# Kernel optimization log

Hardware: AMD Instinct MI355X
Metric: run time of the kernel (lower is better)

## Reference

```python
import jax, jax.numpy as jnp
import numpy as np
from jax import lax

PAD = 10
K = 2 * PAD + 1  # 21
EPS = 1e-8


def _window(x, init, op):
    # sliding KxK window over the last two dims, stride 1, VALID
    return lax.reduce_window(x, init, op, (1, 1, K, K), (1, 1, 1, 1), 'VALID')


def setup_inputs() -> dict:
    key = jax.random.key(0)
    image = jax.random.uniform(key, (16, 3, 1024, 1024), dtype=jnp.float32)
    return {"image": image}


def reference(image):
    # replicate-pad by 2*PAD on each spatial side -> (B, C, H+4p, W+4p)
    padded = jnp.pad(image, ((0, 0), (0, 0), (2 * PAD, 2 * PAD), (2 * PAD, 2 * PAD)), mode='edge')
    # sliding-window min/max, output size (B, C, H+2p, W+2p)
    mn = _window(padded, jnp.inf, lax.min)      # = -maxpool(-padded)
    mx = _window(padded, -jnp.inf, lax.max)
    # Original computes mean over the KxK unfolded windows of
    #   (image - min_w) / (diff_w + eps)
    # which is linear in image:  image * mean(1/(diff+eps)) - mean(min/(diff+eps)).
    a = 1.0 / (mx - mn + EPS)
    b = mn * a
    inv_area = 1.0 / (K * K)
    avg_a = _window(a, 0.0, lax.add) * inv_area  # (B, C, H, W)
    avg_b = _window(b, 0.0, lax.add) * inv_area
    return image * avg_a - avg_b
```

## Files before the change

kernel.cpp:

```cpp
#include <hip/hip_runtime.h>

#define HDIM 1024
#define TILE 32
#define HALO 20
#define MID  52
#define ABW  1044
#define ABP2 1056
#define EPSF 1e-8f
#define INVF ((float)(1.0 / 441.0))

__device__ __forceinline__ void scan8_mm(const float* vm, const float* vx, float2* o) {
    float smn[8], smx[8];
    float amn = vm[20], amx = vx[20];
#pragma unroll
    for (int j = 19; j >= 8; --j) { amn = fminf(amn, vm[j]); amx = fmaxf(amx, vx[j]); }
#pragma unroll
    for (int i = 7; i >= 0; --i) {
        amn = fminf(amn, vm[i]); amx = fmaxf(amx, vx[i]);
        smn[i] = amn; smx[i] = amx;
    }
    float pmn = vm[21], pmx = vx[21];
    o[0] = make_float2(smn[0], smx[0]);
#pragma unroll
    for (int i = 1; i < 8; ++i) {
        o[i] = make_float2(fminf(smn[i], pmn), fmaxf(smx[i], pmx));
        if (i < 7) { pmn = fminf(pmn, vm[21 + i]); pmx = fmaxf(pmx, vx[21 + i]); }
    }
}

#define K1_IMG_PITCH 54
#define K1_HMM_OFF 4536
#define K1_HMM_PITCH 170
#define K1_WORDS 9984

__global__ __launch_bounds__(256, 4) void san_k1(const float* __restrict__ img,
                                                 float2* __restrict__ ab) {
    __shared__ __align__(16) float smem[K1_WORDS];
    const int tid = threadIdx.x;
    const int I0 = blockIdx.x * 32;
    const int J0 = blockIdx.y * 64;
    const float* __restrict__ imc = img + (size_t)blockIdx.z * (HDIM * HDIM);
    float2* __restrict__ abc = ab + (size_t)blockIdx.z * ((size_t)ABW * ABP2);
    const bool xInt = (blockIdx.x > 0) && (blockIdx.x < gridDim.x - 1);

    for (int idx = tid; idx < 84 * 26; idx += 256) {
        int r = idx / 26, c2 = idx - r * 26;
        int gy = min(HDIM - 1, max(0, J0 - HALO + r));
        float2 t;
        if (xInt) {
            t = *(const float2*)(imc + gy * HDIM + (I0 - HALO) + 2 * c2);
        } else {
            int gx0 = min(HDIM - 1, max(0, I0 - HALO + 2 * c2));
            int gx1 = min(HDIM - 1, max(0, I0 - HALO + 2 * c2 + 1));
            t = make_float2(imc[gy * HDIM + gx0], imc[gy * HDIM + gx1]);
        }
        *(float2*)&smem[r * K1_IMG_PITCH + 2 * c2] = t;
    }
    __syncthreads();

    for (int task = tid; task < 336; task += 256) {
        int r = task >> 2, g = task & 3;
        const float2* p = (const float2*)&smem[r * K1_IMG_PITCH + 8 * g];
        float v[28];
#pragma unroll
        for (int k = 0; k < 14; ++k) { float2 t = p[k]; v[2 * k] = t.x; v[2 * k + 1] = t.y; }
        float2 o[8];
        scan8_mm(v, v, o);
#pragma unroll
        for (int t = 0; t < 8; ++t)
            *(float2*)&smem[K1_HMM_OFF + (8 * g + t) * K1_HMM_PITCH + 2 * r] = o[t];
    }
    __syncthreads();

    {
        int i = tid & 31, gj = tid >> 5;
        const float2* p = (const float2*)&smem[K1_HMM_OFF + i * K1_HMM_PITCH + 16 * gj];
        float vm[28], vx[28];
#pragma unroll
        for (int k = 0; k < 28; ++k) { float2 t = p[k]; vm[k] = t.x; vx[k] = t.y; }
        float2 o[8];
        scan8_mm(vm, vx, o);
#pragma unroll
        for (int t = 0; t < 8; ++t) {
            int jj = J0 + 8 * gj + t, ii = I0 + i;
            float mn = o[t].x, d = o[t].y - o[t].x;
            float a, b;
            if (d == 0.0f) {
                a = 1.0f; b = 0.0f;
            } else {
                a = 1.0f / (d + EPSF);
                b = mn * a;
            }
            if (jj < ABW && ii < ABW)
                abc[(size_t)jj * ABP2 + ii] = make_float2(a, b);
        }
    }
}

#define K2_AB_PITCH 108
#define K2_HS_PITCH 106
#define K2_WORDS 5620

__global__ __launch_bounds__(256, 6) void san_k2(const float* __restrict__ img,
                                                 const float2* __restrict__ ab,
                                                 float* __restrict__ out) {
    __shared__ __align__(16) float smem[K2_WORDS];
    const int tid = threadIdx.x;
    const int I0 = blockIdx.x * TILE;
    const int J0 = blockIdx.y * TILE;
    const float* __restrict__ imc = img + (size_t)blockIdx.z * (HDIM * HDIM);
    const float2* __restrict__ abc = ab + (size_t)blockIdx.z * ((size_t)ABW * ABP2);
    float* __restrict__ oc = out + (size_t)blockIdx.z * (HDIM * HDIM);

    const int px_x = I0 + (tid & 31);
    const int px_y0 = J0 + 4 * (tid >> 5);
    float pix[4];
#pragma unroll
    for (int t = 0; t < 4; ++t) pix[t] = imc[(px_y0 + t) * HDIM + px_x];

    for (int idx = tid; idx < 52 * 26; idx += 256) {
        int r = idx / 26, c4 = idx - r * 26;
        const float4* gp = (const float4*)(abc + (size_t)(J0 + r) * ABP2 + I0) + c4;
        *(float4*)&smem[r * K2_AB_PITCH + 4 * c4] = *gp;
    }
    __syncthreads();

    const bool cornerBlk = (blockIdx.x == 0 || blockIdx.x == gridDim.x - 1) &&
                           (blockIdx.y == 0 || blockIdx.y == gridDim.y - 1);
    float fixVal = 0.0f;
    int fixPy = 0, fixPx = 0;
    float hsa[8], hsb[8];
    if (tid < 208) {
        int v = tid >> 2, g = tid & 3;
        const float4* p = (const float4*)&smem[v * K2_AB_PITCH + 16 * g];
        float2 abv[28];
#pragma unroll
        for (int k = 0; k < 14; ++k) {
            float4 q = p[k];
            abv[2 * k]     = make_float2(q.x, q.y);
            abv[2 * k + 1] = make_float2(q.z, q.w);
        }
        float Sa = 0.0f, Sb = 0.0f;
#pragma unroll
        for (int j = 0; j < 21; ++j) { Sa += abv[j].x; Sb += abv[j].y; }
        hsa[0] = Sa; hsb[0] = Sb;
#pragma unroll
        for (int t = 1; t < 8; ++t) {
            Sa += abv[t + 20].x - abv[t - 1].x;
            Sb += abv[t + 20].y - abv[t - 1].y;
            hsa[t] = Sa; hsb[t] = Sb;
        }
    } else if (cornerBlk && tid == 255) {
        fixPy = (blockIdx.y == 0) ? 0 : (TILE - 1);
        fixPx = (blockIdx.x == 0) ? 0 : (TILE - 1);
        int degY = (blockIdx.y == 0) ? 0 : HALO;
        int degX = (blockIdx.x == 0) ? 0 : HALO;
        float pv = imc[(J0 + fixPy) * HDIM + (I0 + fixPx)];
        float aT = 1.0f / EPSF;
        float bT = pv * aT;
        asm volatile("" : "+v"(bT));
        float Sa = 0.0f, Sb = 0.0f;
#pragma unroll 1
        for (int dy = 0; dy < 21; ++dy) {
#pragma unroll 1
            for (int dx = 0; dx < 21; ++dx) {
                const float* c = &smem[(fixPy + dy) * K2_AB_PITCH + 2 * (fixPx + dx)];
                float av = c[0], bv = c[1];
                if (dy == degY && dx == degX) { av = aT; bv = bT; }
                Sa = Sa + av;
                Sb = Sb + bv;
            }
        }
        float avga = Sa * INVF;
        float avgb = Sb * INVF;
        float tq = pv * avga;
        asm volatile("" : "+v"(tq));
        fixVal = tq - avgb;
    }
    __syncthreads();

    if (tid < 208) {
        int v = tid >> 2, g = tid & 3;
        int xp = 9 * g;
#pragma unroll
        for (int t = 0; t < 8; ++t)
            *(float2*)&smem[(xp + t) * K2_HS_PITCH + 2 * v] = make_float2(hsa[t], hsb[t]);
    }
    __syncthreads();

    {
        int x = tid & 31, h = tid >> 5, y0 = 4 * h;
        int xp = 9 * (x >> 3) + (x & 7);
        const float2* p = (const float2*)&smem[xp * K2_HS_PITCH] + y0;
        float2 vv[24];
#pragma unroll
        for (int j = 0; j < 24; ++j) vv[j] = p[j];
        float Sa = 0.0f, Sb = 0.0f;
#pragma unroll
        for (int j = 0; j < 21; ++j) { Sa += vv[j].x; Sb += vv[j].y; }
#pragma unroll
        for (int t = 0; t < 4; ++t) {
            if (t > 0) {
                Sa += vv[t + 20].x - vv[t - 1].x;
                Sb += vv[t + 20].y - vv[t - 1].y;
            }
            float avga = Sa * INVF, avgb = Sb * INVF;
            oc[(px_y0 + t) * HDIM + px_x] = pix[t] * avga - avgb;
        }
    }

    if (cornerBlk) {
        __syncthreads();
        if (tid == 255) oc[(J0 + fixPy) * HDIM + (I0 + fixPx)] = fixVal;
    }
}

#define IMG_PITCH 74
#define REG2 5616
#define HMM_STRIDE 148
#define AB_PITCH 108
#define HS_STRIDE 106
#define SMEM_WORDS 13328

__device__ __forceinline__ void scan14_mm(const float* vm, const float* vx, float2* o) {
    float smn[14], smx[14];
    float amn = vm[20], amx = vx[20];
#pragma unroll
    for (int j = 19; j >= 14; --j) { amn = fminf(amn, vm[j]); amx = fmaxf(amx, vx[j]); }
#pragma unroll
    for (int i = 13; i >= 0; --i) {
        amn = fminf(amn, vm[i]); amx = fmaxf(amx, vx[i]);
        smn[i] = amn; smx[i] = amx;
    }
    float pmn = vm[21], pmx = vx[21];
    o[0] = make_float2(smn[0], smx[0]);
#pragma unroll
    for (int i = 1; i < 14; ++i) {
        o[i] = make_float2(fminf(smn[i], pmn), fmaxf(smx[i], pmx));
        if (i < 13) { pmn = fminf(pmn, vm[21 + i]); pmx = fmaxf(pmx, vx[21 + i]); }
    }
}

__global__ __launch_bounds__(256, 3) void san_fused(const float* __restrict__ img,
                                                    float* __restrict__ out) {
    __shared__ __align__(16) float smem[SMEM_WORDS];
    const int tid = threadIdx.x;
    const int ox0 = blockIdx.x * TILE;
    const int oy0 = blockIdx.y * TILE;
    const float* __restrict__ imc = img + (size_t)blockIdx.z * (HDIM * HDIM);
    float* __restrict__ oc = out + (size_t)blockIdx.z * (HDIM * HDIM);
    const bool xInterior = (blockIdx.x > 0) && (blockIdx.x < gridDim.x - 1);

    for (int idx = tid; idx < 72 * 36; idx += 256) {
        int r = idx / 36, c2 = idx - r * 36;
        int gy = min(HDIM - 1, max(0, oy0 - HALO + r));
        float2 t;
        if (xInterior) {
            t = *(const float2*)(imc + gy * HDIM + (ox0 - HALO) + 2 * c2);
        } else {
            int gx0 = min(HDIM - 1, max(0, ox0 - HALO + 2 * c2));
            int gx1 = min(HDIM - 1, max(0, ox0 - HALO + 2 * c2 + 1));
            t = make_float2(imc[gy * HDIM + gx0], imc[gy * HDIM + gx1]);
        }
        *(float2*)&smem[r * IMG_PITCH + 2 * c2] = t;
    }
    __syncthreads();

    for (int task = tid; task < 288; task += 256) {
        int r = task >> 2, g = task & 3, u0 = 14 * g;
        const float2* p = (const float2*)&smem[r * IMG_PITCH + u0];
        float v[34];
#pragma unroll
        for (int k = 0; k < 17; ++k) { float2 t = p[k]; v[2 * k] = t.x; v[2 * k + 1] = t.y; }
        float2 o[14];
        scan14_mm(v, v, o);
#pragma unroll
        for (int i = 0; i < 14; ++i) {
            int u = u0 + i;
            if (u < MID) *(float2*)&smem[REG2 + u * HMM_STRIDE + 2 * r] = o[i];
        }
    }
    __syncthreads();

    if (tid < 208) {
        int u = tid % MID, v0 = 14 * (tid / MID);
        const float4* p = (const float4*)&smem[REG2 + u * HMM_STRIDE + 2 * v0];
        float vm[34], vx[34];
#pragma unroll
        for (int k = 0; k < 17; ++k) {
            float4 q = p[k];
            vm[2 * k] = q.x; vx[2 * k] = q.y; vm[2 * k + 1] = q.z; vx[2 * k + 1] = q.w;
        }
        float2 o[14];
        scan14_mm(vm, vx, o);
#pragma unroll
        for (int i = 0; i < 14; ++i) {
            int v = v0 + i;
            if (v < MID) {
                float mn = o[i].x, d = o[i].y - o[i].x;
                float a, b;
                if (d == 0.0f) { a = 1.0f; b = 0.0f; }
                else { a = 1.0f / (d + EPSF); b = mn * a; }
                *(float2*)&smem[v * AB_PITCH + 2 * u] = make_float2(a, b);
            }
        }
    }
    __syncthreads();

    const bool cornerBlk = (blockIdx.x == 0 || blockIdx.x == gridDim.x - 1) &&
                           (blockIdx.y == 0 || blockIdx.y == gridDim.y - 1);
    float fixVal = 0.0f;
    int fixPy = 0, fixPx = 0;
    if (tid < 208) {
        int v = tid >> 2, g = tid & 3, xb = 8 * g;
        const float4* p = (const float4*)&smem[v * AB_PITCH + 16 * g];
        float2 ab[28];
#pragma unroll
        for (int k = 0; k < 14; ++k) {
            float4 q = p[k];
            ab[2 * k]     = make_float2(q.x, q.y);
            ab[2 * k + 1] = make_float2(q.z, q.w);
        }
        float Sa = 0.0f, Sb = 0.0f;
#pragma unroll
        for (int j = 0; j < 21; ++j) { Sa += ab[j].x; Sb += ab[j].y; }
        *(float2*)&smem[REG2 + xb * HS_STRIDE + 2 * v] = make_float2(Sa, Sb);
#pragma unroll
        for (int t = 1; t < 8; ++t) {
            Sa += ab[t + 20].x - ab[t - 1].x;
            Sb += ab[t + 20].y - ab[t - 1].y;
            *(float2*)&smem[REG2 + (xb + t) * HS_STRIDE + 2 * v] = make_float2(Sa, Sb);
        }
    } else if (cornerBlk && tid == 255) {
        fixPy = (blockIdx.y == 0) ? 0 : (TILE - 1);
        fixPx = (blockIdx.x == 0) ? 0 : (TILE - 1);
        int degY = (blockIdx.y == 0) ? 0 : HALO;
        int degX = (blockIdx.x == 0) ? 0 : HALO;
        float pv = imc[(oy0 + fixPy) * HDIM + (ox0 + fixPx)];
        float aT = 1.0f / EPSF;
        float bT = pv * aT;
        asm volatile("" : "+v"(bT));
        float Sa = 0.0f, Sb = 0.0f;
#pragma unroll 1
        for (int dy = 0; dy < 21; ++dy) {
#pragma unroll 1
            for (int dx = 0; dx < 21; ++dx) {
                const float* c = &smem[(fixPy + dy) * AB_PITCH + 2 * (fixPx + dx)];
                float av = c[0], bv = c[1];
                if (dy == degY && dx == degX) { av = aT; bv = bT; }
                Sa = Sa + av;
                Sb = Sb + bv;
            }
        }
        float avga = Sa * INVF;
        float avgb = Sb * INVF;
        float tq = pv * avga;
        asm volatile("" : "+v"(tq));
        fixVal = tq - avgb;
    }
    __syncthreads();

    {
        int x = tid & 31, h = tid >> 5, y0 = 4 * h;
        const float2* p = (const float2*)&smem[REG2 + x * HS_STRIDE + 2 * y0];
        float2 vv[24];
#pragma unroll
        for (int j = 0; j < 24; ++j) vv[j] = p[j];
        float Sa = 0.0f, Sb = 0.0f;
#pragma unroll
        for (int j = 0; j < 21; ++j) { Sa += vv[j].x; Sb += vv[j].y; }
#pragma unroll
        for (int t = 0; t < 4; ++t) {
            if (t > 0) {
                Sa += vv[t + 20].x - vv[t - 1].x;
                Sb += vv[t + 20].y - vv[t - 1].y;
            }
            float avga = Sa * INVF, avgb = Sb * INVF;
            int oy = oy0 + y0 + t, ox = ox0 + x;
            float pix = imc[oy * HDIM + ox];
            oc[oy * HDIM + ox] = pix * avga - avgb;
        }
    }

    if (cornerBlk) {
        __syncthreads();
        if (tid == 255) oc[(oy0 + fixPy) * HDIM + (ox0 + fixPx)] = fixVal;
    }
}

extern "C" void kernel_launch(void* const* d_in, const int* in_sizes, int n_in,
                              void* d_out, int out_size, void* d_ws, size_t ws_size,
                              hipStream_t stream) {
    const float* img = (const float*)d_in[0];
    float* out = (float*)d_out;
    int nch = in_sizes[0] / (HDIM * HDIM);
    size_t need = (size_t)nch * ABW * ABP2 * sizeof(float2);
    if (ws_size >= need) {
        float2* ab = (float2*)d_ws;
        dim3 g1(33, 17, nch);
        san_k1<<<g1, dim3(256), 0, stream>>>(img, ab);
        dim3 g2(HDIM / TILE, HDIM / TILE, nch);
        san_k2<<<g2, dim3(256), 0, stream>>>(img, ab, out);
    } else {
        dim3 grid(HDIM / TILE, HDIM / TILE, nch);
        san_fused<<<grid, dim3(256), 0, stream>>>(img, out);
    }
}
```

Measured before the change: 495.8 us.

## Stream global loads directly into registers and shrink LDS in both kernels

Kernel 1 now uses 32x32 tiles, and each thread reads its image row segment straight from global memory into registers for the horizontal min/max scan, dropping the shared-memory image staging pass and one barrier. Kernel 2 likewise loads a/b rows directly from global memory into its horizontal prefix-sum registers and removes one barrier. Its corner-fix computation moves to the thread that owns that pixel, which removes the extra trailing barrier and store. Both kernels use less LDS and raise the occupancy hint to 7, at the cost of redundant global reads across overlapping row segments and a larger grid for kernel 1 with more halo recomputation.

Measured after the change: 869.3 us. 1.75x slower.

```diff
diff --git a/kernel.cpp b/kernel.cpp
--- a/kernel.cpp
+++ b/kernel.cpp
@@ -28,56 +28,50 @@
     }
 }
 
-#define K1_IMG_PITCH 54
-#define K1_HMM_OFF 4536
-#define K1_HMM_PITCH 170
-#define K1_WORDS 9984
-
-__global__ __launch_bounds__(256, 4) void san_k1(const float* __restrict__ img,
+#define K1_PITCH 108
+#define K1_WORDS 3456
+
+__global__ __launch_bounds__(256, 7) void san_k1(const float* __restrict__ img,
                                                  float2* __restrict__ ab) {
     __shared__ __align__(16) float smem[K1_WORDS];
     const int tid = threadIdx.x;
-    const int I0 = blockIdx.x * 32;
-    const int J0 = blockIdx.y * 64;
+    const int I0 = blockIdx.x * TILE;
+    const int J0 = blockIdx.y * TILE;
     const float* __restrict__ imc = img + (size_t)blockIdx.z * (HDIM * HDIM);
     float2* __restrict__ abc = ab + (size_t)blockIdx.z * ((size_t)ABW * ABP2);
-    const bool xInt = (blockIdx.x > 0) && (blockIdx.x < gridDim.x - 1);
-
-    for (int idx = tid; idx < 84 * 26; idx += 256) {
-        int r = idx / 26, c2 = idx - r * 26;
+    const bool xInt = (I0 >= 32) && (I0 <= HDIM - 32);
+
+    if (tid < 208) {
+        int r = tid >> 2, g = tid & 3;
         int gy = min(HDIM - 1, max(0, J0 - HALO + r));
-        float2 t;
+        const float* rowp = imc + (size_t)gy * HDIM;
+        int base = I0 + 8 * g - HALO;
+        float v[28];
         if (xInt) {
-            t = *(const float2*)(imc + gy * HDIM + (I0 - HALO) + 2 * c2);
+            const float2* p2 = (const float2*)(rowp + base);
+#pragma unroll
+            for (int k = 0; k < 14; ++k) { float2 t = p2[k]; v[2 * k] = t.x; v[2 * k + 1] = t.y; }
         } else {
-            int gx0 = min(HDIM - 1, max(0, I0 - HALO + 2 * c2));
-            int gx1 = min(HDIM - 1, max(0, I0 - HALO + 2 * c2 + 1));
-            t = make_float2(imc[gy * HDIM + gx0], imc[gy * HDIM + gx1]);
-        }
-        *(float2*)&smem[r * K1_IMG_PITCH + 2 * c2] = t;
-    }
-    __syncthreads();
-
-    for (int task = tid; task < 336; task += 256) {
-        int r = task >> 2, g = task & 3;
-        const float2* p = (const float2*)&smem[r * K1_IMG_PITCH + 8 * g];
-        float v[28];
-#pragma unroll
-        for (int k = 0; k < 14; ++k) { float2 t = p[k]; v[2 * k] = t.x; v[2 * k + 1] = t.y; }
+#pragma unroll
+            for (int k = 0; k < 28; ++k) v[k] = rowp[min(HDIM - 1, max(0, base + k))];
+        }
         float2 o[8];
         scan8_mm(v, v, o);
 #pragma unroll
         for (int t = 0; t < 8; ++t)
-            *(float2*)&smem[K1_HMM_OFF + (8 * g + t) * K1_HMM_PITCH + 2 * r] = o[t];
-    }
-    __syncthreads();
-
-    {
+            *(float2*)&smem[(8 * g + t) * K1_PITCH + 2 * r] = o[t];
+    }
+    __syncthreads();
+
+    if (tid < 128) {
         int i = tid & 31, gj = tid >> 5;
-        const float2* p = (const float2*)&smem[K1_HMM_OFF + i * K1_HMM_PITCH + 16 * gj];
+        const float4* p4 = (const float4*)&smem[i * K1_PITCH + 16 * gj];
         float vm[28], vx[28];
 #pragma unroll
-        for (int k = 0; k < 28; ++k) { float2 t = p[k]; vm[k] = t.x; vx[k] = t.y; }
+        for (int k = 0; k < 14; ++k) {
+            float4 q = p4[k];
+            vm[2 * k] = q.x; vx[2 * k] = q.y; vm[2 * k + 1] = q.z; vx[2 * k + 1] = q.w;
+        }
         float2 o[8];
         scan8_mm(vm, vx, o);
 #pragma unroll
@@ -97,11 +91,11 @@
     }
 }
 
-#define K2_AB_PITCH 108
-#define K2_HS_PITCH 106
-#define K2_WORDS 5620
-
-__global__ __launch_bounds__(256, 6) void san_k2(const float* __restrict__ img,
+#define K2_PITCH 108
+#define K2_FIXOFF 3456
+#define K2_WORDS 4344
+
+__global__ __launch_bounds__(256, 7) void san_k2(const float* __restrict__ img,
                                                  const float2* __restrict__ ab,
                                                  float* __restrict__ out) {
     __shared__ __align__(16) float smem[K2_WORDS];
@@ -112,92 +106,98 @@
     const float2* __restrict__ abc = ab + (size_t)blockIdx.z * ((size_t)ABW * ABP2);
     float* __restrict__ oc = out + (size_t)blockIdx.z * (HDIM * HDIM);
 
+    const bool cornerBlk = (blockIdx.x == 0 || blockIdx.x == gridDim.x - 1) &&
+                           (blockIdx.y == 0 || blockIdx.y == gridDim.y - 1);
+    const int fixPy = (blockIdx.y == 0) ? 0 : (TILE - 1);
+    const int fixPx = (blockIdx.x == 0) ? 0 : (TILE - 1);
+
     const int px_x = I0 + (tid & 31);
     const int px_y0 = J0 + 4 * (tid >> 5);
     float pix[4];
 #pragma unroll
     for (int t = 0; t < 4; ++t) pix[t] = imc[(px_y0 + t) * HDIM + px_x];
 
-    for (int idx = tid; idx < 52 * 26; idx += 256) {
-        int r = idx / 26, c4 = idx - r * 26;
-        const float4* gp = (const float4*)(abc + (size_t)(J0 + r) * ABP2 + I0) + c4;
-        *(float4*)&smem[r * K2_AB_PITCH + 4 * c4] = *gp;
-    }
-    __syncthreads();
-
-    const bool cornerBlk = (blockIdx.x == 0 || blockIdx.x == gridDim.x - 1) &&
-                           (blockIdx.y == 0 || blockIdx.y == gridDim.y - 1);
-    float fixVal = 0.0f;
-    int fixPy = 0, fixPx = 0;
-    float hsa[8], hsb[8];
     if (tid < 208) {
         int v = tid >> 2, g = tid & 3;
-        const float4* p = (const float4*)&smem[v * K2_AB_PITCH + 16 * g];
-        float2 abv[28];
+        const float4* p4 = (const float4*)(abc + (size_t)(J0 + v) * ABP2 + I0 + 8 * g);
+        float2 lo[7], hi[7];
+        float Sa = 0.0f, Sb = 0.0f;
 #pragma unroll
         for (int k = 0; k < 14; ++k) {
-            float4 q = p[k];
-            abv[2 * k]     = make_float2(q.x, q.y);
-            abv[2 * k + 1] = make_float2(q.z, q.w);
+            float4 q = p4[k];
+            float2 e0 = make_float2(q.x, q.y);
+            float2 e1 = make_float2(q.z, q.w);
+            int i0 = 2 * k, i1 = 2 * k + 1;
+            if (i0 < 7)  lo[i0] = e0;
+            if (i1 < 7)  lo[i1] = e1;
+            if (i0 >= 21) hi[i0 - 21] = e0;
+            if (i1 >= 21) hi[i1 - 21] = e1;
+            if (i0 < 21) { Sa += e0.x; Sb += e0.y; }
+            if (i1 < 21) { Sa += e1.x; Sb += e1.y; }
+        }
+        float hsa[8], hsb[8];
+        hsa[0] = Sa; hsb[0] = Sb;
+#pragma unroll
+        for (int t = 1; t < 8; ++t) {
+            Sa += hi[t - 1].x - lo[t - 1].x;
+            Sb += hi[t - 1].y - lo[t - 1].y;
+            hsa[t] = Sa; hsb[t] = Sb;
+        }
+#pragma unroll
+        for (int t = 0; t < 8; ++t)
+            *(float2*)&smem[(8 * g + t) * K2_PITCH + 2 * v] = make_float2(hsa[t], hsb[t]);
+    } else if (cornerBlk) {
+        int l = tid - 208;
+        for (int idx = l; idx < 441; idx += 48) {
+            int dy = idx / 21, dx = idx - 21 * dy;
+            float2 t = abc[(size_t)(J0 + fixPy + dy) * ABP2 + (I0 + fixPx + dx)];
+            *(float2*)&smem[K2_FIXOFF + 2 * idx] = t;
+        }
+    }
+    __syncthreads();
+
+    {
+        int x = tid & 31, h = tid >> 5;
+        const float4* p4 = (const float4*)&smem[x * K2_PITCH + 8 * h];
+        float2 vv[24];
+#pragma unroll
+        for (int k = 0; k < 12; ++k) {
+            float4 q = p4[k];
+            vv[2 * k]     = make_float2(q.x, q.y);
+            vv[2 * k + 1] = make_float2(q.z, q.w);
         }
         float Sa = 0.0f, Sb = 0.0f;
 #pragma unroll
-        for (int j = 0; j < 21; ++j) { Sa += abv[j].x; Sb += abv[j].y; }
-        hsa[0] = Sa; hsb[0] = Sb;
-#pragma unroll
-        for (int t = 1; t < 8; ++t) {
-            Sa += abv[t + 20].x - abv[t - 1].x;
-            Sb += abv[t + 20].y - abv[t - 1].y;
-            hsa[t] = Sa; hsb[t] = Sb;
-        }
-    } else if (cornerBlk && tid == 255) {
-        fixPy = (blockIdx.y == 0) ? 0 : (TILE - 1);
-        fixPx = (blockIdx.x == 0) ? 0 : (TILE - 1);
-        int degY = (blockIdx.y == 0) ? 0 : HALO;
-        int degX = (blockIdx.x == 0) ? 0 : HALO;
-        float pv = imc[(J0 + fixPy) * HDIM + (I0 + fixPx)];
-        float aT = 1.0f / EPSF;
-        float bT = pv * aT;
-        asm volatile("" : "+v"(bT));
-        float Sa = 0.0f, Sb = 0.0f;
+        for (int j = 0; j < 21; ++j) { Sa += vv[j].x; Sb += vv[j].y; }
+
+        const bool haveFix = cornerBlk && (x == fixPx) && (h == (fixPy >> 2));
+        float fv = 0.0f;
+        if (haveFix) {
+            int degY = (blockIdx.y == 0) ? 0 : HALO;
+            int degX = (blockIdx.x == 0) ? 0 : HALO;
+            float pv = pix[fixPy & 3];
+            float aT = 1.0f / EPSF;
+            float bT = pv * aT;
+            asm volatile("" : "+v"(bT));
+            float Fa = 0.0f, Fb = 0.0f;
 #pragma unroll 1
-        for (int dy = 0; dy < 21; ++dy) {
+            for (int dy = 0; dy < 21; ++dy) {
 #pragma unroll 1
-            for (int dx = 0; dx < 21; ++dx) {
-                const float* c = &smem[(fixPy + dy) * K2_AB_PITCH + 2 * (fixPx + dx)];
-                float av = c[0], bv = c[1];
-                if (dy == degY && dx == degX) { av = aT; bv = bT; }
-                Sa = Sa + av;
-                Sb = Sb + bv;
-            }
-        }
-        float avga = Sa * INVF;
-        float avgb = Sb * INVF;
-        float tq = pv * avga;
-        asm volatile("" : "+v"(tq));
-        fixVal = tq - avgb;
-    }
-    __syncthreads();
-
-    if (tid < 208) {
-        int v = tid >> 2, g = tid & 3;
-        int xp = 9 * g;
-#pragma unroll
-        for (int t = 0; t < 8; ++t)
-            *(float2*)&smem[(xp + t) * K2_HS_PITCH + 2 * v] = make_float2(hsa[t], hsb[t]);
-    }
-    __syncthreads();
-
-    {
-        int x = tid & 31, h = tid >> 5, y0 = 4 * h;
-        int xp = 9 * (x >> 3) + (x & 7);
-        const float2* p = (const float2*)&smem[xp * K2_HS_PITCH] + y0;
-        float2 vv[24];
-#pragma unroll
-        for (int j = 0; j < 24; ++j) vv[j] = p[j];
-        float Sa = 0.0f, Sb = 0.0f;
-#pragma unroll
-        for (int j = 0; j < 21; ++j) { Sa += vv[j].x; Sb += vv[j].y; }
+                for (int dx = 0; dx < 21; ++dx) {
+                    const float* c = &smem[K2_FIXOFF + 2 * (dy * 21 + dx)];
+                    float av = c[0], bv = c[1];
+                    if (dy == degY && dx == degX) { av = aT; bv = bT; }
+                    Fa = Fa + av;
+                    Fb = Fb + bv;
+                }
+            }
+            float avga = Fa * INVF;
+            float avgb = Fb * INVF;
+            float tq = pv * avga;
+            asm volatile("" : "+v"(tq));
+            fv = tq - avgb;
+        }
+
 #pragma unroll
         for (int t = 0; t < 4; ++t) {
             if (t > 0) {
@@ -205,13 +205,10 @@
                 Sb += vv[t + 20].y - vv[t - 1].y;
             }
             float avga = Sa * INVF, avgb = Sb * INVF;
-            oc[(px_y0 + t) * HDIM + px_x] = pix[t] * avga - avgb;
-        }
-    }
-
-    if (cornerBlk) {
-        __syncthreads();
-        if (tid == 255) oc[(J0 + fixPy) * HDIM + (I0 + fixPx)] = fixVal;
+            float val = pix[t] * avga - avgb;
+            if (haveFix && t == (fixPy & 3)) val = fv;
+            oc[(px_y0 + t) * HDIM + px_x] = val;
+        }
     }
 }
 
@@ -397,7 +394,7 @@
     size_t need = (size_t)nch * ABW * ABP2 * sizeof(float2);
     if (ws_size >= need) {
         float2* ab = (float2*)d_ws;
-        dim3 g1(33, 17, nch);
+        dim3 g1(33, 33, nch);
         san_k1<<<g1, dim3(256), 0, stream>>>(img, ab);
         dim3 g2(HDIM / TILE, HDIM / TILE, nch);
         san_k2<<<g2, dim3(256), 0, stream>>>(img, ab, out);
```
